# Kernel tuning notes

Hardware: AMD Instinct MI355X
Metric: run time of the kernel (lower is better)

Reference implementation:

```python
import jax, jax.numpy as jnp
import numpy as np

N = 50000          # nodes
E = 800000         # edges (COO)
IN_CH = 128
H1, H2, OUT = 200, 100, 2   # 100*out, 50*out, out with out_channels=2
EPS = 1e-12
DROP_P = 0.1


def setup_inputs() -> dict:
    key = jax.random.key(0)
    ks = jax.random.split(key, 6)
    x = jax.random.normal(ks[0], (N, IN_CH), dtype=jnp.float32)
    edge_index = jax.random.randint(ks[1], (2, E), 0, N)
    W1 = jax.random.normal(ks[2], (IN_CH, H1), dtype=jnp.float32) / np.sqrt(IN_CH)
    W2 = jax.random.normal(ks[3], (H1, H2), dtype=jnp.float32) / np.sqrt(H1)
    W3 = jax.random.normal(ks[4], (H2, OUT), dtype=jnp.float32) / np.sqrt(H2)
    beta1 = jnp.float32(1.0)
    beta2 = jnp.float32(1.0)
    beta3 = jnp.float32(1.0)
    return dict(x=x, edge_index=edge_index, W1=W1, W2=W2, W3=W3,
                beta1=beta1, beta2=beta2, beta3=beta3)


def _agnn_layer(x, W, beta, src, dst):
    # project in -> out channels, then AGNN cosine-attention propagation
    h = x @ W                                               # [N, D]
    hn = h / jnp.maximum(jnp.linalg.norm(h, axis=-1, keepdims=True), EPS)
    a = beta * jnp.sum(hn[src] * hn[dst], axis=-1)          # [E'] edge logits
    amax = jax.ops.segment_max(a, dst, num_segments=N)      # stable segment softmax
    amax = jnp.where(jnp.isfinite(amax), amax, 0.0)
    e = jnp.exp(a - amax[dst])
    denom = jax.ops.segment_sum(e, dst, num_segments=N)
    alpha = e / jnp.maximum(denom[dst], EPS)
    return jax.ops.segment_sum(h[src] * alpha[:, None], dst, num_segments=N)


def _dropout(k, x, p=DROP_P):
    keep = jax.random.bernoulli(k, 1.0 - p, x.shape)
    return jnp.where(keep, x / (1.0 - p), 0.0)


def reference(x, edge_index, W1, W2, W3, beta1, beta2, beta3):
    src, dst = edge_index[0], edge_index[1]
    loop = jnp.arange(N)                                    # self-loops (AGNNConv default)
    src = jnp.concatenate([src, loop])
    dst = jnp.concatenate([dst, loop])
    k1, k2 = jax.random.split(jax.random.key(42))
    h = jax.nn.relu(_agnn_layer(x, W1, beta1, src, dst))
    h = _dropout(k1, h)
    h = jax.nn.relu(_agnn_layer(h, W2, beta2, src, dst))
    h = _dropout(k2, h)
    h = jax.nn.relu(_agnn_layer(h, W3, beta3, src, dst))
    return h
```

## Files before the change

### kernel.cpp

```cpp
#include <hip/hip_runtime.h>
#include <hip/hip_bf16.h>

#define NN 50000
#define NE 800000
#define TE 850000
#define EPSN 1e-12f


#define H_OFF    0ull
#define A_OFF    40000000ull
#define H3_OFF   80000000ull
#define RINV_OFF 80400000ull
#define OFFS_OFF 80600000ull
#define DEG_OFF  80800016ull
#define CURS_OFF 81000016ull
#define ESRC_OFF 81200016ull
#define CHNK_OFF 84600016ull
#define RINV3_OFF 84600272ull

__host__ __device__ inline void tf20(unsigned k0, unsigned k1, unsigned& x0, unsigned& x1) {
  unsigned ks2 = k0 ^ k1 ^ 0x1BD11BDAu;
  x0 += k0; x1 += k1;
#define TFR(r) { x0 += x1; x1 = ((x1 << (r)) | (x1 >> (32 - (r)))) ^ x0; }
  TFR(13) TFR(15) TFR(26) TFR(6)
  x0 += k1;  x1 += ks2 + 1u;
  TFR(17) TFR(29) TFR(16) TFR(24)
  x0 += ks2; x1 += k0 + 2u;
  TFR(13) TFR(15) TFR(26) TFR(6)
  x0 += k0;  x1 += k1 + 3u;
  TFR(17) TFR(29) TFR(16) TFR(24)
  x0 += k1;  x1 += ks2 + 4u;
  TFR(13) TFR(15) TFR(26) TFR(6)
  x0 += ks2; x1 += k0 + 5u;
#undef TFR
}

__device__ __forceinline__ float dropf(float val, unsigned k0, unsigned k1, unsigned i) {
  unsigned x0 = 0u, x1 = i;
  tf20(k0, k1, x0, x1);
  unsigned bits = x0 ^ x1;
  float u = __uint_as_float((bits >> 9) | 0x3F800000u) - 1.0f;
  return (u < 0.9f) ? val * (1.0f / 0.9f) : 0.0f;
}

__device__ __forceinline__ float wave_sum(float x) {
  x += __shfl_xor(x, 32); x += __shfl_xor(x, 16); x += __shfl_xor(x, 8);
  x += __shfl_xor(x, 4);  x += __shfl_xor(x, 2);  x += __shfl_xor(x, 1);
  return x;
}

__global__ __launch_bounds__(256) void csr_zero_kernel(int* __restrict__ p, int n) {
  int stride = gridDim.x * 256;
  for (int i = blockIdx.x * 256 + threadIdx.x; i < n; i += stride) p[i] = 0;
}

__global__ __launch_bounds__(256) void csr_hist_kernel(const int* __restrict__ ei, int* __restrict__ deg) {
  int e = blockIdx.x * 256 + threadIdx.x;
  if (e >= TE) return;
  int d = (e < NE) ? ei[NE + e] : (e - NE);
  atomicAdd(&deg[d], 1);
}

__global__ __launch_bounds__(256) void csr_scan1_kernel(const int* __restrict__ deg,
                                                        int* __restrict__ offs,
                                                        int* __restrict__ chunk) {
  __shared__ int lds[8];
  int t = threadIdx.x;
  int base = blockIdx.x * 1024 + t * 4;
  int d[4];
#pragma unroll
  for (int j = 0; j < 4; j++) d[j] = (base + j < NN) ? deg[base + j] : 0;
  int ts = d[0] + d[1] + d[2] + d[3];
  int lane = t & 63, wave = t >> 6;
  int inc = ts;
#pragma unroll
  for (int sh = 1; sh < 64; sh <<= 1) { int u = __shfl_up(inc, sh); if (lane >= sh) inc += u; }
  if (lane == 63) lds[wave] = inc;
  __syncthreads();
  if (t == 0) { int s = 0; for (int w = 0; w < 4; w++) { int x = lds[w]; lds[w] = s; s += x; } lds[4] = s; }
  __syncthreads();
  int p = lds[wave] + inc - ts;
#pragma unroll
  for (int j = 0; j < 4; j++) { if (base + j < NN) offs[base + j] = p; p += d[j]; }
  if (t == 255) chunk[blockIdx.x] = lds[4];
}

__global__ __launch_bounds__(64) void csr_scan2_kernel(int* __restrict__ chunk) {
  int t = threadIdx.x;
  int v = (t < 49) ? chunk[t] : 0;
  int inc = v;
#pragma unroll
  for (int sh = 1; sh < 64; sh <<= 1) { int u = __shfl_up(inc, sh); if (t >= sh) inc += u; }
  if (t < 49) chunk[t] = inc - v;
}

__global__ __launch_bounds__(256) void csr_scan3_kernel(int* __restrict__ offs,
                                                        const int* __restrict__ chunk,
                                                        int* __restrict__ curs) {
  int i = blockIdx.x * 256 + threadIdx.x;
  if (i < NN) {
    int val = offs[i] + chunk[i >> 10];
    offs[i] = val;
    curs[i] = val;
  }
  if (i == 0) offs[NN] = TE;
}

__global__ __launch_bounds__(256) void csr_scatter_kernel(const int* __restrict__ ei,
                                                          int* __restrict__ curs,
                                                          int* __restrict__ esrc) {
  int e = blockIdx.x * 256 + threadIdx.x;
  if (e >= TE) return;
  int s, d;
  if (e < NE) { s = ei[e]; d = ei[NE + e]; } else { s = d = e - NE; }
  int pos = atomicAdd(&curs[d], 1);
  esrc[pos] = s;
}

template<int K, int KT, int NLP, int N>
__device__ __forceinline__ void gemm_body(const float* __restrict__ A,
                                          const float* __restrict__ W,
                                          float* __restrict__ H,
                                          float* __restrict__ RINV, int M) {
  constexpr int CPT = NLP / 8, KTP = KT + 1, NV = N / 4, QV = CPT / 4;
  __shared__ float As[64 * KTP];
  __shared__ float Ws[KT * NLP];
  const float4* A4 = (const float4*)A;
  const float4* W4 = (const float4*)W;
  const float4* Ws4 = (const float4*)Ws;

  int t = threadIdx.x, rgrp = t >> 3, cg = t & 7;
  int row0 = blockIdx.x * 64;
  float acc0[CPT], acc1[CPT];
#pragma unroll
  for (int j = 0; j < CPT; j++) { acc0[j] = 0.f; acc1[j] = 0.f; }

  for (int k0 = 0; k0 < K; k0 += KT) {
    __syncthreads();
    for (int idx = t; idx < 64 * (KT / 4); idx += 256) {
      int r = idx / (KT / 4), cq = idx - r * (KT / 4);
      int gr = row0 + r;
      float4 v = (gr < M) ? A4[(size_t)gr * (K / 4) + (k0 / 4) + cq]
                          : make_float4(0.f, 0.f, 0.f, 0.f);
      float* dst = &As[r * KTP + cq * 4];
      dst[0] = v.x; dst[1] = v.y; dst[2] = v.z; dst[3] = v.w;
    }
    for (int idx = t; idx < KT * NV; idx += 256) {
      int kk = idx / NV, cq = idx - kk * NV;
      *(float4*)&Ws[kk * NLP + cq * 4] = W4[(size_t)(k0 + kk) * NV + cq];
    }
    if (NLP > N) {
      for (int idx = t; idx < KT * ((NLP - N) / 4); idx += 256) {
        int kk = idx / ((NLP - N) / 4), cq = idx - kk * ((NLP - N) / 4);
        *(float4*)&Ws[kk * NLP + N + cq * 4] = make_float4(0.f, 0.f, 0.f, 0.f);
      }
    }
    __syncthreads();
#pragma unroll
    for (int kk = 0; kk < KT; kk++) {
      float a0 = As[(rgrp * 2) * KTP + kk];
      float a1 = As[(rgrp * 2 + 1) * KTP + kk];
#pragma unroll
      for (int q = 0; q < QV; q++) {
        float4 wv = Ws4[(kk * NLP + cg * CPT) / 4 + q];
        acc0[q * 4 + 0] = fmaf(a0, wv.x, acc0[q * 4 + 0]);
        acc0[q * 4 + 1] = fmaf(a0, wv.y, acc0[q * 4 + 1]);
        acc0[q * 4 + 2] = fmaf(a0, wv.z, acc0[q * 4 + 2]);
        acc0[q * 4 + 3] = fmaf(a0, wv.w, acc0[q * 4 + 3]);
        acc1[q * 4 + 0] = fmaf(a1, wv.x, acc1[q * 4 + 0]);
        acc1[q * 4 + 1] = fmaf(a1, wv.y, acc1[q * 4 + 1]);
        acc1[q * 4 + 2] = fmaf(a1, wv.z, acc1[q * 4 + 2]);
        acc1[q * 4 + 3] = fmaf(a1, wv.w, acc1[q * 4 + 3]);
      }
    }
  }

  int r0 = row0 + rgrp * 2;
#pragma unroll
  for (int rr = 0; rr < 2; rr++) {
    int gr = r0 + rr;
    const float* acc = rr ? acc1 : acc0;
    float ss = 0.f;
#pragma unroll
    for (int j = 0; j < CPT; j++) {
      float v = acc[j];
      ss += v * v;
      int c = cg * CPT + j;
      if (gr < M && c < N) H[(size_t)gr * N + c] = v;
    }
    ss += __shfl_xor(ss, 1); ss += __shfl_xor(ss, 2); ss += __shfl_xor(ss, 4);
    if (cg == 0 && gr < M) RINV[gr] = 1.0f / fmaxf(sqrtf(ss), EPSN);
  }
}

__global__ __launch_bounds__(256) void gemm1_kernel(const float* A, const float* W,
                                                    float* H, float* RINV, int M) {
  gemm_body<128, 32, 224, 200>(A, W, H, RINV, M);
}
__global__ __launch_bounds__(256) void gemm2_kernel(const float* A, const float* W,
                                                    float* H, float* RINV, int M) {
  gemm_body<200, 40, 128, 100>(A, W, H, RINV, M);
}

template<int D, int VEC, bool DROP, bool G3FUSE>
__device__ __forceinline__ void attn_body(const float* __restrict__ H,
                                          const float* __restrict__ RINV,
                                          const int* __restrict__ OFFS,
                                          const int* __restrict__ ESRC,
                                          const float* __restrict__ BETA,
                                          float* __restrict__ OUT,
                                          const float* __restrict__ W3g,
                                          float* __restrict__ H3,
                                          float* __restrict__ RINVO,
                                          unsigned k0, unsigned k1) {
  constexpr int NL = D / VEC;
  int v = blockIdx.x * 4 + (threadIdx.x >> 6);
  int lane = threadIdx.x & 63;
  bool act = lane < NL;
  const float* hrow = H + (size_t)v * D + lane * VEC;
  float hd[VEC];
#pragma unroll
  for (int j = 0; j < VEC; j++) hd[j] = 0.f;
  if (act) {
    if (VEC == 4) { float4 tv = *(const float4*)hrow; hd[0] = tv.x; hd[1] = tv.y; hd[2] = tv.z; hd[3] = tv.w; }
    else          { float2 tv = *(const float2*)hrow; hd[0] = tv.x; hd[1] = tv.y; }
  }
  float bd = BETA[0] * RINV[v];
  int e0 = OFFS[v], e1 = OFFS[v + 1];

  float s = 0.0f;
  float acc[VEC];
#pragma unroll
  for (int j = 0; j < VEC; j++) acc[j] = 0.0f;

  int idx = e0;
  for (; idx + 4 <= e1; idx += 4) {
    int   u[4];
    float r[4], dt[4], hs[4][VEC];
#pragma unroll
    for (int m = 0; m < 4; m++) u[m] = ESRC[idx + m];
#pragma unroll
    for (int m = 0; m < 4; m++) r[m] = RINV[u[m]];
#pragma unroll
    for (int m = 0; m < 4; m++) {
      const float* p = H + (size_t)u[m] * D + lane * VEC;
#pragma unroll
      for (int j = 0; j < VEC; j++) hs[m][j] = 0.f;
      if (act) {
        if (VEC == 4) { float4 a = *(const float4*)p; hs[m][0] = a.x; hs[m][1] = a.y; hs[m][2] = a.z; hs[m][3] = a.w; }
        else          { float2 a = *(const float2*)p; hs[m][0] = a.x; hs[m][1] = a.y; }
      }
    }
#pragma unroll
    for (int m = 0; m < 4; m++) {
      float d = 0.f;
#pragma unroll
      for (int j = 0; j < VEC; j++) d = fmaf(hd[j], hs[m][j], d);
      dt[m] = wave_sum(d);
    }
#pragma unroll
    for (int m = 0; m < 4; m++) {
      float w = __expf(bd * dt[m] * r[m]);
      s += w;
#pragma unroll
      for (int j = 0; j < VEC; j++) acc[j] = fmaf(w, hs[m][j], acc[j]);
    }
  }
  for (; idx < e1; ++idx) {
    int u0 = ESRC[idx];
    float r0 = RINV[u0];
    const float* p0 = H + (size_t)u0 * D + lane * VEC;
    float h0[VEC];
#pragma unroll
    for (int j = 0; j < VEC; j++) h0[j] = 0.f;
    if (act) {
      if (VEC == 4) { float4 a = *(const float4*)p0; h0[0] = a.x; h0[1] = a.y; h0[2] = a.z; h0[3] = a.w; }
      else          { float2 a = *(const float2*)p0; h0[0] = a.x; h0[1] = a.y; }
    }
    float d0 = 0.f;
#pragma unroll
    for (int j = 0; j < VEC; j++) d0 = fmaf(hd[j], h0[j], d0);
    d0 = wave_sum(d0);
    float w0 = __expf(bd * d0 * r0);
    s += w0;
#pragma unroll
    for (int j = 0; j < VEC; j++) acc[j] = fmaf(w0, h0[j], acc[j]);
  }

  float rs = 1.0f / fmaxf(s, EPSN);
  float o[VEC];
#pragma unroll
  for (int j = 0; j < VEC; j++) {
    float val = acc[j] * rs;
    val = (val <= 0.0f) ? 0.0f : val;
    if (DROP) val = dropf(val, k0, k1, (unsigned)(v * D + lane * VEC + j));
    o[j] = act ? val : 0.0f;
  }
  if (G3FUSE) {
    float p0 = 0.f, p1 = 0.f;
    if (act) {
      float w00 = W3g[4 * lane], w01 = W3g[4 * lane + 1];
      float w10 = W3g[4 * lane + 2], w11 = W3g[4 * lane + 3];
      p0 = o[0] * w00 + o[1] * w10;
      p1 = o[0] * w01 + o[1] * w11;
    }
    p0 = wave_sum(p0); p1 = wave_sum(p1);
    if (lane == 0) {
      H3[2 * v] = p0; H3[2 * v + 1] = p1;
      RINVO[v] = 1.0f / fmaxf(sqrtf(p0 * p0 + p1 * p1), EPSN);
    }
  } else if (act) {
    float* orow = OUT + (size_t)v * D + lane * VEC;
    if (VEC == 4) *(float4*)orow = make_float4(o[0], o[1], o[2], o[3]);
    else          *(float2*)orow = make_float2(o[0], o[1]);
  }
}

__global__ __launch_bounds__(256) void attn1_kernel(const float* H, const float* RINV,
                                                    const int* OFFS, const int* ESRC,
                                                    const float* BETA, float* OUT,
                                                    unsigned k0, unsigned k1) {
  attn_body<200, 4, true, false>(H, RINV, OFFS, ESRC, BETA, OUT, nullptr, nullptr, nullptr, k0, k1);
}
__global__ __launch_bounds__(256) void attn2g3_kernel(const float* H, const float* RINV,
                                                      const int* OFFS, const int* ESRC,
                                                      const float* BETA, const float* W3g,
                                                      float* H3, float* RINV3,
                                                      unsigned k0, unsigned k1) {
  attn_body<100, 2, true, true>(H, RINV, OFFS, ESRC, BETA, nullptr, W3g, H3, RINV3, k0, k1);
}

__global__ __launch_bounds__(256) void attn3_kernel(const float* __restrict__ H3,
                                                    const float* __restrict__ RINV3,
                                                    const int* __restrict__ OFFS,
                                                    const int* __restrict__ ESRC,
                                                    const float* __restrict__ BETA,
                                                    float* __restrict__ out) {
  int v = blockIdx.x * 4 + (threadIdx.x >> 6);
  int lane = threadIdx.x & 63;
  float bd = BETA[0] * RINV3[v];
  float h0 = H3[2 * v], h1 = H3[2 * v + 1];
  int e0 = OFFS[v], e1 = OFFS[v + 1];
  float s = 0.f, a0 = 0.f, a1 = 0.f;
  for (int idx = e0 + lane; idx < e1; idx += 64) {
    int u = ESRC[idx];
    float s0 = H3[2 * u], s1 = H3[2 * u + 1];
    float w = __expf(bd * (h0 * s0 + h1 * s1) * RINV3[u]);
    s += w; a0 = fmaf(w, s0, a0); a1 = fmaf(w, s1, a1);
  }
  s = wave_sum(s); a0 = wave_sum(a0); a1 = wave_sum(a1);
  if (lane == 0) {
    float rs = 1.0f / fmaxf(s, EPSN);
    float o0 = a0 * rs, o1 = a1 * rs;
    out[2 * v]     = (o0 <= 0.0f) ? 0.0f : o0;
    out[2 * v + 1] = (o1 <= 0.0f) ? 0.0f : o1;
  }
}

extern "C" void kernel_launch(void* const* d_in, const int* in_sizes, int n_in,
                              void* d_out, int out_size, void* d_ws, size_t ws_size,
                              hipStream_t stream) {
  const float* X  = (const float*)d_in[0];
  const int*   EI = (const int*)d_in[1];
  const float* W1 = (const float*)d_in[2];
  const float* W2 = (const float*)d_in[3];
  const float* W3 = (const float*)d_in[4];
  const float* B1 = (const float*)d_in[5];
  const float* B2 = (const float*)d_in[6];
  const float* B3 = (const float*)d_in[7];

  char* ws = (char*)d_ws;
  float* H     = (float*)(ws + H_OFF);
  float* A     = (float*)(ws + A_OFF);
  float* H3    = (float*)(ws + H3_OFF);
  float* RINV  = (float*)(ws + RINV_OFF);
  float* RINV3 = (float*)(ws + RINV3_OFF);
  int* OFFS    = (int*)(ws + OFFS_OFF);
  int* DEG     = (int*)(ws + DEG_OFF);
  int* CURS    = (int*)(ws + CURS_OFF);
  int* ESRC    = (int*)(ws + ESRC_OFF);
  int* CHNK    = (int*)(ws + CHNK_OFF);

  unsigned k1a = 0u, k1b = 0u; tf20(0u, 42u, k1a, k1b);
  unsigned k2a = 0u, k2b = 1u; tf20(0u, 42u, k2a, k2b);

  csr_zero_kernel<<<64, 256, 0, stream>>>(DEG, NN);
  csr_hist_kernel<<<(TE + 255) / 256, 256, 0, stream>>>(EI, DEG);
  csr_scan1_kernel<<<49, 256, 0, stream>>>(DEG, OFFS, CHNK);
  csr_scan2_kernel<<<1, 64, 0, stream>>>(CHNK);
  csr_scan3_kernel<<<196, 256, 0, stream>>>(OFFS, CHNK, CURS);
  csr_scatter_kernel<<<(TE + 255) / 256, 256, 0, stream>>>(EI, CURS, ESRC);

  const int gb = (NN + 63) / 64;
  const int ab = NN / 4;

  gemm1_kernel<<<gb, 256, 0, stream>>>(X, W1, H, RINV, NN);
  attn1_kernel<<<ab, 256, 0, stream>>>(H, RINV, OFFS, ESRC, B1, A, k1a, k1b);
  gemm2_kernel<<<gb, 256, 0, stream>>>(A, W2, H, RINV, NN);
  attn2g3_kernel<<<ab, 256, 0, stream>>>(H, RINV, OFFS, ESRC, B2, W3, H3, RINV3, k2a, k2b);
  attn3_kernel<<<ab, 256, 0, stream>>>(H3, RINV3, OFFS, ESRC, B3, (float*)d_out);
}
```

Measured before the change: 557.8 us.

## Rewrite first-layer GEMM to keep weight columns in registers

Replaces the shared-memory tiled GEMM for layer 1 with a kernel where each lane holds one full 128-entry weight column in registers and streams rows of x directly from global memory (uniform broadcast loads), computing 8 rows at a time. Row-norm partials are reduced with wave sums into shared memory and combined at the end. The aim is to remove the padded 224-column tiling and shared-memory traffic. In exchange it uses very high register pressure (128 weight registers), leaves 56 of 256 lanes idle, and relies on scalar global loads of A with no explicit reuse. gemm2 keeps the old tiled code, now inlined.

```diff
diff --git a/kernel.cpp b/kernel.cpp
--- a/kernel.cpp
+++ b/kernel.cpp
@@ -117,11 +117,66 @@
   esrc[pos] = s;
 }
 
-template<int K, int KT, int NLP, int N>
-__device__ __forceinline__ void gemm_body(const float* __restrict__ A,
-                                          const float* __restrict__ W,
-                                          float* __restrict__ H,
-                                          float* __restrict__ RINV, int M) {
+__global__ __launch_bounds__(256, 3) void gemm1_kernel(const float* __restrict__ A,
+                                                       const float* __restrict__ W,
+                                                       float* __restrict__ H,
+                                                       float* __restrict__ RINV, int M) {
+  __shared__ float Ws[64 * 200];
+  __shared__ float ssp[4 * 64];
+  int t = threadIdx.x, w = t >> 6, lane = t & 63;
+  bool act = lane < 50;
+  int col = 50 * w + lane;
+  int r0 = blockIdx.x * 64;
+  int nrow = M - r0; if (nrow > 64) nrow = 64;
+
+  float wreg[128];
+#pragma unroll
+  for (int kc = 0; kc < 2; kc++) {
+    __syncthreads();
+    const float4* Wg = (const float4*)(W + kc * 64 * 200);
+    for (int idx = t; idx < 3200; idx += 256) ((float4*)Ws)[idx] = Wg[idx];
+    __syncthreads();
+#pragma unroll
+    for (int kk = 0; kk < 64; kk++)
+      wreg[kc * 64 + kk] = act ? Ws[kk * 200 + col] : 0.f;
+  }
+
+  for (int r = 0; r < nrow; r += 8) {
+    const float* A0 = A + (size_t)(r0 + r) * 128;
+    float c0 = 0.f, c1 = 0.f, c2 = 0.f, c3 = 0.f, c4 = 0.f, c5 = 0.f, c6 = 0.f, c7 = 0.f;
+#pragma unroll
+    for (int k = 0; k < 128; k++) {
+      float wv = wreg[k];
+      c0 = fmaf(A0[k],        wv, c0);
+      c1 = fmaf(A0[128 + k],  wv, c1);
+      c2 = fmaf(A0[256 + k],  wv, c2);
+      c3 = fmaf(A0[384 + k],  wv, c3);
+      c4 = fmaf(A0[512 + k],  wv, c4);
+      c5 = fmaf(A0[640 + k],  wv, c5);
+      c6 = fmaf(A0[768 + k],  wv, c6);
+      c7 = fmaf(A0[896 + k],  wv, c7);
+    }
+#define G1FIN(i, ci) {                                              \
+      if (act) H[(size_t)(r0 + r + i) * 200 + col] = ci;            \
+      float ps = wave_sum(ci * ci);                                 \
+      if (lane == 0) ssp[w * 64 + r + i] = ps; }
+    G1FIN(0, c0) G1FIN(1, c1) G1FIN(2, c2) G1FIN(3, c3)
+    G1FIN(4, c4) G1FIN(5, c5) G1FIN(6, c6) G1FIN(7, c7)
+#undef G1FIN
+  }
+
+  __syncthreads();
+  if (t < nrow) {
+    float ss = ssp[t] + ssp[64 + t] + ssp[128 + t] + ssp[192 + t];
+    RINV[r0 + t] = 1.0f / fmaxf(sqrtf(ss), EPSN);
+  }
+}
+
+__global__ __launch_bounds__(256) void gemm2_kernel(const float* __restrict__ A,
+                                                    const float* __restrict__ W,
+                                                    float* __restrict__ H,
+                                                    float* __restrict__ RINV, int M) {
+  constexpr int K = 200, KT = 40, NLP = 128, N = 100;
   constexpr int CPT = NLP / 8, KTP = KT + 1, NV = N / 4, QV = CPT / 4;
   __shared__ float As[64 * KTP];
   __shared__ float Ws[KT * NLP];
@@ -149,11 +204,9 @@
       int kk = idx / NV, cq = idx - kk * NV;
       *(float4*)&Ws[kk * NLP + cq * 4] = W4[(size_t)(k0 + kk) * NV + cq];
     }
-    if (NLP > N) {
-      for (int idx = t; idx < KT * ((NLP - N) / 4); idx += 256) {
-        int kk = idx / ((NLP - N) / 4), cq = idx - kk * ((NLP - N) / 4);
-        *(float4*)&Ws[kk * NLP + N + cq * 4] = make_float4(0.f, 0.f, 0.f, 0.f);
-      }
+    for (int idx = t; idx < KT * ((NLP - N) / 4); idx += 256) {
+      int kk = idx / ((NLP - N) / 4), cq = idx - kk * ((NLP - N) / 4);
+      *(float4*)&Ws[kk * NLP + N + cq * 4] = make_float4(0.f, 0.f, 0.f, 0.f);
     }
     __syncthreads();
 #pragma unroll
@@ -191,15 +244,6 @@
     ss += __shfl_xor(ss, 1); ss += __shfl_xor(ss, 2); ss += __shfl_xor(ss, 4);
     if (cg == 0 && gr < M) RINV[gr] = 1.0f / fmaxf(sqrtf(ss), EPSN);
   }
-}
-
-__global__ __launch_bounds__(256) void gemm1_kernel(const float* A, const float* W,
-                                                    float* H, float* RINV, int M) {
-  gemm_body<128, 32, 224, 200>(A, W, H, RINV, M);
-}
-__global__ __launch_bounds__(256) void gemm2_kernel(const float* A, const float* W,
-                                                    float* H, float* RINV, int M) {
-  gemm_body<200, 40, 128, 100>(A, W, H, RINV, M);
 }
 
 template<int D, int VEC, bool DROP, bool G3FUSE>
```

Result: slower. 869.0 us (+55.8%).
